# Optimization experiments

Hardware: AMD Instinct MI355X
Metric: run time of the kernel (lower is better)

Reference implementation:

```python
import jax, jax.numpy as jnp
import numpy as np

B, T, D, H = 4, 4096, 1024, 64

def setup_inputs() -> dict:
    key = jax.random.key(0)
    k1, k2, k3, k4 = jax.random.split(key, 4)
    x = jax.random.normal(k1, (B, T, D), dtype=jnp.float32)
    Wk = jax.random.normal(k2, (D, H), dtype=jnp.float32) * (D ** -0.5)
    Wq = jax.random.normal(k3, (D, H), dtype=jnp.float32) * (D ** -0.5)
    Wv = jax.random.normal(k4, (D, H), dtype=jnp.float32) * (D ** -0.5)
    return {"x": x, "Wk": Wk, "Wq": Wq, "Wv": Wv}

def reference(x, Wk, Wq, Wv):
    # single-head causal self-attention (dropout inactive: training=False)
    k = x @ Wk  # [B,T,H]
    q = x @ Wq  # [B,T,H]
    v = x @ Wv  # [B,T,H]
    scale = jnp.float32(1.0) / jnp.sqrt(jnp.float32(H))
    wei = jnp.einsum('bth,bsh->bts', q, k) * scale  # [B,T,T]
    t = x.shape[1]
    causal = jnp.tril(jnp.ones((t, t), dtype=bool))[None, :, :]
    wei = jnp.where(causal, wei, jnp.float32(-jnp.inf))
    wei = jax.nn.softmax(wei, axis=-1)
    out = jnp.einsum('bts,bsh->bth', wei, v)  # [B,T,H]
    return out
```

## Files before the change

### kernel.cpp

```cpp
#include <hip/hip_runtime.h>

typedef __bf16 bf16_t;
typedef __bf16 bf16x8 __attribute__((ext_vector_type(8)));
typedef __bf16 bf16x4 __attribute__((ext_vector_type(4)));
typedef float  f32x4  __attribute__((ext_vector_type(4)));
typedef float  f32x16 __attribute__((ext_vector_type(16)));

#define B_  4
#define T_  4096
#define H_  64
#define BT  (B_*T_)

#define QSCALE 0.1803368801111204f

#define NSLOT_PB 1088
#define NSLOT    4352

#define WS_KFR  0x0000000u
#define WS_QFR  0x0200000u
#define WS_VFR  0x0400000u
#define WS_WTF  0x0600000u
#define WS_POUT 0x0680000u
#define WS_PL   0x1780000u

#define MFMA16(a,b,c) __builtin_amdgcn_mfma_f32_16x16x32_bf16((a),(b),(c),0,0,0)
#define MFMA32(a,b,c) __builtin_amdgcn_mfma_f32_32x32x16_bf16((a),(b),(c),0,0,0)

__device__ __forceinline__ unsigned pk2(float a, float b) {
  union { __bf16 h[2]; unsigned u; } u_;
  u_.h[0] = (__bf16)a; u_.h[1] = (__bf16)b;
  return u_.u;
}

__device__ __forceinline__ f32x16 zero16() {
  f32x16 z;
#pragma unroll
  for (int i = 0; i < 16; ++i) z[i] = 0.f;
  return z;
}

__global__ __launch_bounds__(128) void wtrans_kernel(
    const float* __restrict__ Wk, const float* __restrict__ Wq,
    const float* __restrict__ Wv, bf16_t* __restrict__ WTf) {
  __shared__ float lw[64][17];
  int bid = blockIdx.x;
  int nt = bid >> 4;
  int kc = bid & 15;
  int w  = nt >> 2;
  const float* W = (w == 0) ? Wk : (w == 1) ? Wq : Wv;
  float sc = (w == 1) ? QSCALE : 1.0f;
  int nl0 = (nt & 3) * 16;

  int t = threadIdx.x;
  int rr = t >> 1;
  int c0 = (t & 1) * 8;
  const float* src = W + (size_t)(kc*64 + rr)*64 + nl0 + c0;
  float4 v0 = *reinterpret_cast<const float4*>(src);
  float4 v1 = *reinterpret_cast<const float4*>(src + 4);
  lw[rr][c0+0] = v0.x; lw[rr][c0+1] = v0.y; lw[rr][c0+2] = v0.z; lw[rr][c0+3] = v0.w;
  lw[rr][c0+4] = v1.x; lw[rr][c0+5] = v1.y; lw[rr][c0+6] = v1.z; lw[rr][c0+7] = v1.w;
  __syncthreads();

  int kk   = t >> 6;
  int lane = t & 63;
  int col  = lane & 15;
  int g    = lane >> 4;
  bf16x8 o;
#pragma unroll
  for (int e = 0; e < 8; ++e) o[e] = (bf16_t)(lw[kk*32 + g*8 + e][col] * sc);
  *reinterpret_cast<bf16x8*>(WTf + ((size_t)bid*2 + kk)*512 + lane*8) = o;
}

__global__ __launch_bounds__(256) void proj_kernel(
    const float* __restrict__ x, const bf16_t* __restrict__ WTf,
    bf16_t* __restrict__ kfr, bf16_t* __restrict__ qfr, bf16_t* __restrict__ vfr) {
  __shared__ __bf16 xs[2][16][72];
  int tid  = threadIdx.x;
  int wv   = tid >> 6;
  int lane = tid & 63;
  int col  = lane & 15;
  int g    = lane >> 4;
  int m0   = blockIdx.x * 16;

  f32x4 zero4 = {0.f, 0.f, 0.f, 0.f};
  f32x4 acc[3] = {zero4, zero4, zero4};

  int srow = tid >> 4;
  int scol = (tid & 15) * 4;
  const float* xrow = x + (size_t)(m0 + srow)*1024 + scol;

  float4 a0 = *reinterpret_cast<const float4*>(xrow);
  float4 b0 = *reinterpret_cast<const float4*>(xrow + 64);
  {
    bf16x4 pk = { (bf16_t)a0.x,(bf16_t)a0.y,(bf16_t)a0.z,(bf16_t)a0.w };
    *reinterpret_cast<bf16x4*>(&xs[0][srow][scol]) = pk;
  }

  const bf16_t* wtb = WTf + lane*8;

  for (int t = 0; t < 16; ++t) {
    __syncthreads();
    int cur = t & 1;
    if (t + 2 < 16) {
      const float* p = xrow + (t+2)*64;
      if ((t & 1) == 0) a0 = *reinterpret_cast<const float4*>(p);
      else              b0 = *reinterpret_cast<const float4*>(p);
    }
#pragma unroll
    for (int kk = 0; kk < 2; ++kk) {
      int ko = kk*32 + g*8;
      bf16x8 f0 = *(const bf16x8*)&xs[cur][col][ko];
#pragma unroll
      for (int nti = 0; nti < 3; ++nti) {
        int nt = wv*3 + nti;
        bf16x8 bfr = *(const bf16x8*)(wtb + ((size_t)(nt*16 + t)*2 + kk)*512);
        acc[nti] = MFMA16(f0, bfr, acc[nti]);
      }
    }
    if (t + 1 < 16) {
      float4 sv = ((t & 1) == 0) ? b0 : a0;
      bf16x4 pk = { (bf16_t)sv.x,(bf16_t)sv.y,(bf16_t)sv.z,(bf16_t)sv.w };
      *reinterpret_cast<bf16x4*>(&xs[cur^1][srow][scol]) = pk;
    }
  }
  int row0 = m0 + 4*g;
#pragma unroll
  for (int nti = 0; nti < 3; ++nti) {
    int n = wv*48 + nti*16 + col;
    f32x4 v = acc[nti];
    if (n < 128) {
      int h = n & 63;
      bf16_t* base = (n < 64) ? kfr : qfr;
#pragma unroll
      for (int r = 0; r < 4; ++r) {
        int t2 = row0 + r;
        size_t idx = (size_t)((t2>>6)*8 + ((t2>>5)&1)*4 + (h>>4))*512
                   + (size_t)((t2&31) + ((h>>3)&1)*32)*8 + (h&7);
        base[idx] = (bf16_t)v[r];
      }
    } else {
      int h = n - 128;
      size_t idx = (size_t)((row0>>6)*8 + ((h>>5)&1)*4 + ((row0>>4)&3))*512
                 + (size_t)((h&31) + ((row0>>3)&1)*32)*8 + (row0&7);
      bf16x4 pk = { (bf16_t)v[0], (bf16_t)v[1], (bf16_t)v[2], (bf16_t)v[3] };
      *reinterpret_cast<bf16x4*>(&vfr[idx]) = pk;
    }
  }
}

__global__ __launch_bounds__(64) void attn_kernel(
    const bf16_t* __restrict__ qfr, const bf16_t* __restrict__ kfr,
    const bf16_t* __restrict__ vfr, bf16_t* __restrict__ pout,
    float* __restrict__ pl) {
  int l  = threadIdx.x;
  int ql = l & 31;
  int hi = l >> 5;

  int bidx = blockIdx.x;
  int b = bidx / NSLOT_PB;
  int s = bidx - b * NSLOT_PB;
  s = NSLOT_PB - 1 - s;
  int a = 0;
#pragma unroll
  for (int aa = 1; aa < 16; ++aa) if (4*aa*(aa+1) <= s) a = aa;
  int r2 = s - 4*a*(a+1);
  int qd = r2 / (a+1);
  int c  = r2 - qd*(a+1);
  int jt = 8*a + qd;
  int slot = b*NSLOT_PB + s;

  int q0    = jt << 5;
  int kv_lo = c << 8;
  int kv_hi = min(kv_lo + 256, q0 + 32);
  int ntiles = (kv_hi - kv_lo + 63) >> 6;
  int qg = q0 + ql;

  const bf16_t* qb = qfr + (size_t)((b*T_ + q0) >> 6)*4096
                   + (size_t)((q0 >> 5) & 1)*2048 + l*8;
  bf16x8 qf0 = *(const bf16x8*)(qb);
  bf16x8 qf1 = *(const bf16x8*)(qb + 512);
  bf16x8 qf2 = *(const bf16x8*)(qb + 1024);
  bf16x8 qf3 = *(const bf16x8*)(qb + 1536);

  const bf16_t* kfb = kfr + (size_t)(b*T_)*64 + l*8;
  const bf16_t* vfb = vfr + (size_t)(b*T_)*64 + l*8;

  bf16x8 kA0,kA1,kA2,kA3, kB0,kB1,kB2,kB3;
#define LOADK(kvt_) do { const bf16_t* kp_ = kfb + (size_t)(kvt_)*64;          \
    kA0=*(const bf16x8*)(kp_);        kA1=*(const bf16x8*)(kp_+512);           \
    kA2=*(const bf16x8*)(kp_+1024);   kA3=*(const bf16x8*)(kp_+1536);          \
    kB0=*(const bf16x8*)(kp_+2048);   kB1=*(const bf16x8*)(kp_+2560);          \
    kB2=*(const bf16x8*)(kp_+3072);   kB3=*(const bf16x8*)(kp_+3584); } while(0)

  LOADK(kv_lo);

  f32x16 oA = zero16(), oB = zero16();
  float l_ = 0.f;

  for (int t = 0; t < ntiles; ++t) {
    int kvt = kv_lo + t*64;
    const bf16_t* vp = vfb + (size_t)kvt*64;
    bf16x8 vA0 = *(const bf16x8*)(vp);
    bf16x8 vA1 = *(const bf16x8*)(vp + 512);
    bf16x8 vA2 = *(const bf16x8*)(vp + 1024);
    bf16x8 vA3 = *(const bf16x8*)(vp + 1536);
    bf16x8 vB0 = *(const bf16x8*)(vp + 2048);
    bf16x8 vB1 = *(const bf16x8*)(vp + 2560);
    bf16x8 vB2 = *(const bf16x8*)(vp + 3072);
    bf16x8 vB3 = *(const bf16x8*)(vp + 3584);

    f32x16 sA = zero16(), sB = zero16();
    __builtin_amdgcn_s_setprio(1);
    sA = MFMA32(kA0, qf0, sA); sB = MFMA32(kB0, qf0, sB);
    sA = MFMA32(kA1, qf1, sA); sB = MFMA32(kB1, qf1, sB);
    sA = MFMA32(kA2, qf2, sA); sB = MFMA32(kB2, qf2, sB);
    sA = MFMA32(kA3, qf3, sA); sB = MFMA32(kB3, qf3, sB);
    __builtin_amdgcn_s_setprio(0);

    if (t + 1 < ntiles) LOADK(kvt + 64);

    if (kvt + 63 > q0) {
#pragma unroll
      for (int r = 0; r < 16; ++r) {
        int kvo = kvt + (r&3) + 8*(r>>2) + 4*hi;
        if (kvo > qg)      sA[r] = -1e30f;
        if (kvo + 32 > qg) sB[r] = -1e30f;
      }
    }

    float pA[16], pB[16];
    float ts = 0.f;
#pragma unroll
    for (int r = 0; r < 16; ++r) { pA[r] = exp2f(sA[r]); ts += pA[r]; }
#pragma unroll
    for (int r = 0; r < 16; ++r) { pB[r] = exp2f(sB[r]); ts += pB[r]; }
    l_ += ts + __shfl_xor(ts, 32);

    bf16x8 p0, p1, p2, p3;
#define MKSLICES(P, F0, F1) do {                                               \
    unsigned w0 = pk2(P[0],P[1]),   w1 = pk2(P[2],P[3]);                       \
    unsigned w2 = pk2(P[4],P[5]),   w3 = pk2(P[6],P[7]);                       \
    unsigned w4 = pk2(P[8],P[9]),   w5 = pk2(P[10],P[11]);                     \
    unsigned w6 = pk2(P[12],P[13]), w7 = pk2(P[14],P[15]);                     \
    unsigned x0 = (unsigned)__shfl_xor((int)w0,32);                            \
    unsigned x1 = (unsigned)__shfl_xor((int)w1,32);                            \
    unsigned x2 = (unsigned)__shfl_xor((int)w2,32);                            \
    unsigned x3 = (unsigned)__shfl_xor((int)w3,32);                            \
    unsigned x4 = (unsigned)__shfl_xor((int)w4,32);                            \
    unsigned x5 = (unsigned)__shfl_xor((int)w5,32);                            \
    unsigned x6 = (unsigned)__shfl_xor((int)w6,32);                            \
    unsigned x7 = (unsigned)__shfl_xor((int)w7,32);                            \
    union { unsigned d[4]; bf16x8 v; } u0_, u1_;                               \
    u0_.d[0] = hi ? x2 : w0;  u0_.d[1] = hi ? x3 : w1;                         \
    u0_.d[2] = hi ? w2 : x0;  u0_.d[3] = hi ? w3 : x1;                         \
    u1_.d[0] = hi ? x6 : w4;  u1_.d[1] = hi ? x7 : w5;                         \
    u1_.d[2] = hi ? w6 : x4;  u1_.d[3] = hi ? w7 : x5;                         \
    F0 = u0_.v; F1 = u1_.v; } while(0)
    MKSLICES(pA, p0, p1);
    MKSLICES(pB, p2, p3);

    __builtin_amdgcn_s_setprio(1);
    oA = MFMA32(vA0, p0, oA); oB = MFMA32(vB0, p0, oB);
    oA = MFMA32(vA1, p1, oA); oB = MFMA32(vB1, p1, oB);
    oA = MFMA32(vA2, p2, oA); oB = MFMA32(vB2, p2, oB);
    oA = MFMA32(vA3, p3, oA); oB = MFMA32(vB3, p3, oB);
    __builtin_amdgcn_s_setprio(0);
  }

  bf16_t* po = pout + (size_t)slot * 2048;
#pragma unroll
  for (int r = 0; r < 16; ++r) {
    int h = (r&3) + 8*(r>>2) + 4*hi;
    po[h*32 + ql]      = (bf16_t)oA[r];
    po[(h+32)*32 + ql] = (bf16_t)oB[r];
  }
  if (l < 32) pl[(size_t)slot*32 + l] = l_;
}

__global__ __launch_bounds__(256) void combine_kernel(
    const bf16_t* __restrict__ pout, const float* __restrict__ pl,
    float* __restrict__ out) {
  int blk = blockIdx.x;
  int b  = blk >> 7;
  int jt = blk & 127;
  int tid = threadIdx.x;
  int wv = tid >> 6;
  int l  = tid & 63;
  int a  = jt >> 3;
  int nch = a + 1;
  int slot0 = b*NSLOT_PB + 4*a*(a+1) + (jt & 7)*(a+1);

  float oacc[8], lacc[8];
#pragma unroll
  for (int q = 0; q < 8; ++q) { oacc[q] = 0.f; lacc[q] = 0.f; }
  for (int c2 = 0; c2 < nch; ++c2) {
    const bf16_t* pp = pout + (size_t)(slot0 + c2)*2048 + l*32 + wv*8;
    bf16x8 o8 = *(const bf16x8*)pp;
    const float* plc = pl + (size_t)(slot0 + c2)*32 + wv*8;
#pragma unroll
    for (int q = 0; q < 8; ++q) { oacc[q] += (float)o8[q]; lacc[q] += plc[q]; }
  }
  float* op = out + ((size_t)b*T_ + (size_t)jt*32 + wv*8)*64 + l;
#pragma unroll
  for (int q = 0; q < 8; ++q) op[(size_t)q*64] = oacc[q] / lacc[q];
}

extern "C" void kernel_launch(void* const* d_in, const int* in_sizes, int n_in,
                              void* d_out, int out_size, void* d_ws, size_t ws_size,
                              hipStream_t stream) {
  (void)in_sizes; (void)n_in; (void)out_size; (void)ws_size;
  const float* x  = (const float*)d_in[0];
  const float* Wk = (const float*)d_in[1];
  const float* Wq = (const float*)d_in[2];
  const float* Wv = (const float*)d_in[3];
  char* ws = (char*)d_ws;
  bf16_t* kfr  = (bf16_t*)(ws + WS_KFR);
  bf16_t* qfr  = (bf16_t*)(ws + WS_QFR);
  bf16_t* vfr  = (bf16_t*)(ws + WS_VFR);
  bf16_t* WTf  = (bf16_t*)(ws + WS_WTF);
  bf16_t* pout = (bf16_t*)(ws + WS_POUT);
  float*  pl   = (float*)(ws + WS_PL);
  float*  outp = (float*)d_out;

  hipLaunchKernelGGL(wtrans_kernel,  dim3(192),   dim3(128), 0, stream, Wk, Wq, Wv, WTf);
  hipLaunchKernelGGL(proj_kernel,    dim3(1024),  dim3(256), 0, stream, x, WTf, kfr, qfr, vfr);
  hipLaunchKernelGGL(attn_kernel,    dim3(NSLOT), dim3(64),  0, stream, qfr, kfr, vfr, pout, pl);
  hipLaunchKernelGGL(combine_kernel, dim3(512),   dim3(256), 0, stream, pout, pl, outp);
}
```

Baseline: 65.57 us.

## Fuse four kernels into one cooperative persistent kernel with grid syncs

Merges weight transpose, projection, attention and combine into a single cooperative kernel of 512 blocks separated by grid-wide barriers, removing three kernel launch gaps. The projection now computes 32 rows per block with prefetched weight fragments, and attention runs four waves per block looping over slots, with V loads software-pipelined one tile ahead. Risks include grid-sync cost, lower parallelism for attention (2048 waves over 4352 slots, causing tail imbalance), and register pressure from the launch bound of two blocks per CU. A fallback path launches the separate kernels if the cooperative launch fails.

```diff
diff --git a/kernel.cpp b/kernel.cpp
--- a/kernel.cpp
+++ b/kernel.cpp
@@ -1,4 +1,7 @@
 #include <hip/hip_runtime.h>
+#include <hip/hip_cooperative_groups.h>
+
+namespace cg = cooperative_groups;
 
 typedef __bf16 bf16_t;
 typedef __bf16 bf16x8 __attribute__((ext_vector_type(8)));
@@ -15,6 +18,7 @@
 
 #define NSLOT_PB 1088
 #define NSLOT    4352
+#define NWAVES   2048
 
 #define WS_KFR  0x0000000u
 #define WS_QFR  0x0200000u
@@ -26,6 +30,8 @@
 #define MFMA16(a,b,c) __builtin_amdgcn_mfma_f32_16x16x32_bf16((a),(b),(c),0,0,0)
 #define MFMA32(a,b,c) __builtin_amdgcn_mfma_f32_32x32x16_bf16((a),(b),(c),0,0,0)
 
+#define SMEM_BYTES 9216
+
 __device__ __forceinline__ unsigned pk2(float a, float b) {
   union { __bf16 h[2]; unsigned u; } u_;
   u_.h[0] = (__bf16)a; u_.h[1] = (__bf16)b;
@@ -39,11 +45,11 @@
   return z;
 }
 
-__global__ __launch_bounds__(128) void wtrans_kernel(
+__device__ void phase_wtrans(int bid, char* smem,
     const float* __restrict__ Wk, const float* __restrict__ Wq,
     const float* __restrict__ Wv, bf16_t* __restrict__ WTf) {
-  __shared__ float lw[64][17];
-  int bid = blockIdx.x;
+  if (bid >= 192) return;
+  float (*lw)[17] = (float (*)[17])smem;
   int nt = bid >> 4;
   int kc = bid & 15;
   int w  = nt >> 2;
@@ -52,191 +58,218 @@
   int nl0 = (nt & 3) * 16;
 
   int t = threadIdx.x;
-  int rr = t >> 1;
-  int c0 = (t & 1) * 8;
-  const float* src = W + (size_t)(kc*64 + rr)*64 + nl0 + c0;
-  float4 v0 = *reinterpret_cast<const float4*>(src);
-  float4 v1 = *reinterpret_cast<const float4*>(src + 4);
-  lw[rr][c0+0] = v0.x; lw[rr][c0+1] = v0.y; lw[rr][c0+2] = v0.z; lw[rr][c0+3] = v0.w;
-  lw[rr][c0+4] = v1.x; lw[rr][c0+5] = v1.y; lw[rr][c0+6] = v1.z; lw[rr][c0+7] = v1.w;
+  int rr = t >> 2, c0 = (t & 3) * 4;
+  float4 v = *reinterpret_cast<const float4*>(W + (size_t)(kc*64 + rr)*64 + nl0 + c0);
+  lw[rr][c0+0] = v.x; lw[rr][c0+1] = v.y; lw[rr][c0+2] = v.z; lw[rr][c0+3] = v.w;
   __syncthreads();
-
-  int kk   = t >> 6;
-  int lane = t & 63;
-  int col  = lane & 15;
-  int g    = lane >> 4;
-  bf16x8 o;
-#pragma unroll
-  for (int e = 0; e < 8; ++e) o[e] = (bf16_t)(lw[kk*32 + g*8 + e][col] * sc);
-  *reinterpret_cast<bf16x8*>(WTf + ((size_t)bid*2 + kk)*512 + lane*8) = o;
-}
-
-__global__ __launch_bounds__(256) void proj_kernel(
+  if (t < 128) {
+    int kk = t >> 6, lane = t & 63, col = lane & 15, g = lane >> 4;
+    bf16x8 o;
+#pragma unroll
+    for (int e = 0; e < 8; ++e) o[e] = (bf16_t)(lw[kk*32 + g*8 + e][col] * sc);
+    *reinterpret_cast<bf16x8*>(WTf + ((size_t)(nt*16 + kc)*2 + kk)*512 + lane*8) = o;
+  }
+}
+
+__device__ void phase_proj(int bid, char* smem,
     const float* __restrict__ x, const bf16_t* __restrict__ WTf,
     bf16_t* __restrict__ kfr, bf16_t* __restrict__ qfr, bf16_t* __restrict__ vfr) {
-  __shared__ __bf16 xs[2][16][72];
+  typedef __bf16 (*xs_t)[32][72];
+  xs_t xs = (xs_t)smem;
   int tid  = threadIdx.x;
   int wv   = tid >> 6;
   int lane = tid & 63;
   int col  = lane & 15;
   int g    = lane >> 4;
-  int m0   = blockIdx.x * 16;
+  int m0   = bid * 32;
 
   f32x4 zero4 = {0.f, 0.f, 0.f, 0.f};
-  f32x4 acc[3] = {zero4, zero4, zero4};
-
-  int srow = tid >> 4;
-  int scol = (tid & 15) * 4;
+  f32x4 acc[2][3];
+#pragma unroll
+  for (int i = 0; i < 2; ++i)
+#pragma unroll
+    for (int j = 0; j < 3; ++j) acc[i][j] = zero4;
+
+  int srow = tid >> 3;
+  int scol = (tid & 7) * 8;
   const float* xrow = x + (size_t)(m0 + srow)*1024 + scol;
 
   float4 a0 = *reinterpret_cast<const float4*>(xrow);
+  float4 a1 = *reinterpret_cast<const float4*>(xrow + 4);
   float4 b0 = *reinterpret_cast<const float4*>(xrow + 64);
+  float4 b1 = *reinterpret_cast<const float4*>(xrow + 68);
   {
-    bf16x4 pk = { (bf16_t)a0.x,(bf16_t)a0.y,(bf16_t)a0.z,(bf16_t)a0.w };
-    *reinterpret_cast<bf16x4*>(&xs[0][srow][scol]) = pk;
+    bf16x8 pk = { (bf16_t)a0.x,(bf16_t)a0.y,(bf16_t)a0.z,(bf16_t)a0.w,
+                  (bf16_t)a1.x,(bf16_t)a1.y,(bf16_t)a1.z,(bf16_t)a1.w };
+    *reinterpret_cast<bf16x8*>(&xs[0][srow][scol]) = pk;
   }
 
   const bf16_t* wtb = WTf + lane*8;
-
+  bf16x8 bcur[6], bnxt[6];
+#pragma unroll
+  for (int kk = 0; kk < 2; ++kk)
+#pragma unroll
+    for (int nti = 0; nti < 3; ++nti)
+      bcur[kk*3+nti] = *(const bf16x8*)(wtb + ((size_t)((wv*3+nti)*16 + 0)*2 + kk)*512);
+
+#pragma unroll
   for (int t = 0; t < 16; ++t) {
     __syncthreads();
     int cur = t & 1;
     if (t + 2 < 16) {
       const float* p = xrow + (t+2)*64;
-      if ((t & 1) == 0) a0 = *reinterpret_cast<const float4*>(p);
-      else              b0 = *reinterpret_cast<const float4*>(p);
+      if ((t & 1) == 0) { a0 = *reinterpret_cast<const float4*>(p);
+                          a1 = *reinterpret_cast<const float4*>(p + 4); }
+      else              { b0 = *reinterpret_cast<const float4*>(p);
+                          b1 = *reinterpret_cast<const float4*>(p + 4); }
+    }
+    if (t + 1 < 16) {
+#pragma unroll
+      for (int kk = 0; kk < 2; ++kk)
+#pragma unroll
+        for (int nti = 0; nti < 3; ++nti)
+          bnxt[kk*3+nti] = *(const bf16x8*)(wtb + ((size_t)((wv*3+nti)*16 + (t+1))*2 + kk)*512);
     }
 #pragma unroll
     for (int kk = 0; kk < 2; ++kk) {
       int ko = kk*32 + g*8;
-      bf16x8 f0 = *(const bf16x8*)&xs[cur][col][ko];
+      bf16x8 f0 = *(const bf16x8*)&xs[cur][ 0 + col][ko];
+      bf16x8 f1 = *(const bf16x8*)&xs[cur][16 + col][ko];
 #pragma unroll
       for (int nti = 0; nti < 3; ++nti) {
-        int nt = wv*3 + nti;
-        bf16x8 bfr = *(const bf16x8*)(wtb + ((size_t)(nt*16 + t)*2 + kk)*512);
-        acc[nti] = MFMA16(f0, bfr, acc[nti]);
+        acc[0][nti] = MFMA16(f0, bcur[kk*3+nti], acc[0][nti]);
+        acc[1][nti] = MFMA16(f1, bcur[kk*3+nti], acc[1][nti]);
       }
     }
     if (t + 1 < 16) {
-      float4 sv = ((t & 1) == 0) ? b0 : a0;
-      bf16x4 pk = { (bf16_t)sv.x,(bf16_t)sv.y,(bf16_t)sv.z,(bf16_t)sv.w };
-      *reinterpret_cast<bf16x4*>(&xs[cur^1][srow][scol]) = pk;
-    }
-  }
-  int row0 = m0 + 4*g;
-#pragma unroll
-  for (int nti = 0; nti < 3; ++nti) {
-    int n = wv*48 + nti*16 + col;
-    f32x4 v = acc[nti];
-    if (n < 128) {
-      int h = n & 63;
-      bf16_t* base = (n < 64) ? kfr : qfr;
-#pragma unroll
-      for (int r = 0; r < 4; ++r) {
-        int t2 = row0 + r;
-        size_t idx = (size_t)((t2>>6)*8 + ((t2>>5)&1)*4 + (h>>4))*512
-                   + (size_t)((t2&31) + ((h>>3)&1)*32)*8 + (h&7);
-        base[idx] = (bf16_t)v[r];
+      bf16x8 pk;
+      if ((t & 1) == 0)
+        pk = bf16x8{ (bf16_t)b0.x,(bf16_t)b0.y,(bf16_t)b0.z,(bf16_t)b0.w,
+                     (bf16_t)b1.x,(bf16_t)b1.y,(bf16_t)b1.z,(bf16_t)b1.w };
+      else
+        pk = bf16x8{ (bf16_t)a0.x,(bf16_t)a0.y,(bf16_t)a0.z,(bf16_t)a0.w,
+                     (bf16_t)a1.x,(bf16_t)a1.y,(bf16_t)a1.z,(bf16_t)a1.w };
+      *reinterpret_cast<bf16x8*>(&xs[cur^1][srow][scol]) = pk;
+    }
+#pragma unroll
+    for (int i = 0; i < 6; ++i) bcur[i] = bnxt[i];
+  }
+#pragma unroll
+  for (int mt = 0; mt < 2; ++mt) {
+    int row0 = m0 + mt*16 + 4*g;
+#pragma unroll
+    for (int nti = 0; nti < 3; ++nti) {
+      int n = wv*48 + nti*16 + col;
+      f32x4 v = acc[mt][nti];
+      if (n < 128) {
+        int h = n & 63;
+        bf16_t* base = (n < 64) ? kfr : qfr;
+#pragma unroll
+        for (int r = 0; r < 4; ++r) {
+          int t2 = row0 + r;
+          size_t idx = (size_t)((t2>>6)*8 + ((t2>>5)&1)*4 + (h>>4))*512
+                     + (size_t)((t2&31) + ((h>>3)&1)*32)*8 + (h&7);
+          base[idx] = (bf16_t)v[r];
+        }
+      } else {
+        int h = n - 128;
+        size_t idx = (size_t)((row0>>6)*8 + ((h>>5)&1)*4 + ((row0>>4)&3))*512
+                   + (size_t)((h&31) + ((row0>>3)&1)*32)*8 + (row0&7);
+        bf16x4 pk = { (bf16_t)v[0], (bf16_t)v[1], (bf16_t)v[2], (bf16_t)v[3] };
+        *reinterpret_cast<bf16x4*>(&vfr[idx]) = pk;
       }
-    } else {
-      int h = n - 128;
-      size_t idx = (size_t)((row0>>6)*8 + ((h>>5)&1)*4 + ((row0>>4)&3))*512
-                 + (size_t)((h&31) + ((row0>>3)&1)*32)*8 + (row0&7);
-      bf16x4 pk = { (bf16_t)v[0], (bf16_t)v[1], (bf16_t)v[2], (bf16_t)v[3] };
-      *reinterpret_cast<bf16x4*>(&vfr[idx]) = pk;
-    }
-  }
-}
-
-__global__ __launch_bounds__(64) void attn_kernel(
+    }
+  }
+}
+
+__device__ void phase_attn(int bid,
     const bf16_t* __restrict__ qfr, const bf16_t* __restrict__ kfr,
     const bf16_t* __restrict__ vfr, bf16_t* __restrict__ pout,
     float* __restrict__ pl) {
-  int l  = threadIdx.x;
-  int ql = l & 31;
-  int hi = l >> 5;
-
-  int bidx = blockIdx.x;
-  int b = bidx / NSLOT_PB;
-  int s = bidx - b * NSLOT_PB;
-  s = NSLOT_PB - 1 - s;
-  int a = 0;
-#pragma unroll
-  for (int aa = 1; aa < 16; ++aa) if (4*aa*(aa+1) <= s) a = aa;
-  int r2 = s - 4*a*(a+1);
-  int qd = r2 / (a+1);
-  int c  = r2 - qd*(a+1);
-  int jt = 8*a + qd;
-  int slot = b*NSLOT_PB + s;
-
-  int q0    = jt << 5;
-  int kv_lo = c << 8;
-  int kv_hi = min(kv_lo + 256, q0 + 32);
-  int ntiles = (kv_hi - kv_lo + 63) >> 6;
-  int qg = q0 + ql;
-
-  const bf16_t* qb = qfr + (size_t)((b*T_ + q0) >> 6)*4096
-                   + (size_t)((q0 >> 5) & 1)*2048 + l*8;
-  bf16x8 qf0 = *(const bf16x8*)(qb);
-  bf16x8 qf1 = *(const bf16x8*)(qb + 512);
-  bf16x8 qf2 = *(const bf16x8*)(qb + 1024);
-  bf16x8 qf3 = *(const bf16x8*)(qb + 1536);
-
-  const bf16_t* kfb = kfr + (size_t)(b*T_)*64 + l*8;
-  const bf16_t* vfb = vfr + (size_t)(b*T_)*64 + l*8;
-
-  bf16x8 kA0,kA1,kA2,kA3, kB0,kB1,kB2,kB3;
+  int tid = threadIdx.x;
+  int wv  = tid >> 6;
+  int l   = tid & 63;
+  int ql  = l & 31;
+  int hi  = l >> 5;
+
+  for (int si = bid*4 + wv; si < NSLOT; si += NWAVES) {
+    int b = si / NSLOT_PB;
+    int s = si - b * NSLOT_PB;
+    s = NSLOT_PB - 1 - s;
+    int a = 0;
+#pragma unroll
+    for (int aa = 1; aa < 16; ++aa) if (4*aa*(aa+1) <= s) a = aa;
+    int r2 = s - 4*a*(a+1);
+    int qd = r2 / (a+1);
+    int c  = r2 - qd*(a+1);
+    int jt = 8*a + qd;
+    int slot = b*NSLOT_PB + s;
+
+    int q0    = jt << 5;
+    int kv_lo = c << 8;
+    int kv_hi = min(kv_lo + 256, q0 + 32);
+    int ntiles = (kv_hi - kv_lo + 63) >> 6;
+    int qg = q0 + ql;
+
+    const bf16_t* qb = qfr + (size_t)((b*T_ + q0) >> 6)*4096
+                     + (size_t)((q0 >> 5) & 1)*2048 + l*8;
+    bf16x8 qf0 = *(const bf16x8*)(qb);
+    bf16x8 qf1 = *(const bf16x8*)(qb + 512);
+    bf16x8 qf2 = *(const bf16x8*)(qb + 1024);
+    bf16x8 qf3 = *(const bf16x8*)(qb + 1536);
+
+    const bf16_t* kfb = kfr + (size_t)(b*T_)*64 + l*8;
+    const bf16_t* vfb = vfr + (size_t)(b*T_)*64 + l*8;
+
+    bf16x8 kA0,kA1,kA2,kA3, kB0,kB1,kB2,kB3;
+    bf16x8 vA0,vA1,vA2,vA3, vB0,vB1,vB2,vB3;
 #define LOADK(kvt_) do { const bf16_t* kp_ = kfb + (size_t)(kvt_)*64;          \
     kA0=*(const bf16x8*)(kp_);        kA1=*(const bf16x8*)(kp_+512);           \
     kA2=*(const bf16x8*)(kp_+1024);   kA3=*(const bf16x8*)(kp_+1536);          \
     kB0=*(const bf16x8*)(kp_+2048);   kB1=*(const bf16x8*)(kp_+2560);          \
     kB2=*(const bf16x8*)(kp_+3072);   kB3=*(const bf16x8*)(kp_+3584); } while(0)
-
-  LOADK(kv_lo);
-
-  f32x16 oA = zero16(), oB = zero16();
-  float l_ = 0.f;
-
-  for (int t = 0; t < ntiles; ++t) {
-    int kvt = kv_lo + t*64;
-    const bf16_t* vp = vfb + (size_t)kvt*64;
-    bf16x8 vA0 = *(const bf16x8*)(vp);
-    bf16x8 vA1 = *(const bf16x8*)(vp + 512);
-    bf16x8 vA2 = *(const bf16x8*)(vp + 1024);
-    bf16x8 vA3 = *(const bf16x8*)(vp + 1536);
-    bf16x8 vB0 = *(const bf16x8*)(vp + 2048);
-    bf16x8 vB1 = *(const bf16x8*)(vp + 2560);
-    bf16x8 vB2 = *(const bf16x8*)(vp + 3072);
-    bf16x8 vB3 = *(const bf16x8*)(vp + 3584);
-
-    f32x16 sA = zero16(), sB = zero16();
-    __builtin_amdgcn_s_setprio(1);
-    sA = MFMA32(kA0, qf0, sA); sB = MFMA32(kB0, qf0, sB);
-    sA = MFMA32(kA1, qf1, sA); sB = MFMA32(kB1, qf1, sB);
-    sA = MFMA32(kA2, qf2, sA); sB = MFMA32(kB2, qf2, sB);
-    sA = MFMA32(kA3, qf3, sA); sB = MFMA32(kB3, qf3, sB);
-    __builtin_amdgcn_s_setprio(0);
-
-    if (t + 1 < ntiles) LOADK(kvt + 64);
-
-    if (kvt + 63 > q0) {
-#pragma unroll
-      for (int r = 0; r < 16; ++r) {
-        int kvo = kvt + (r&3) + 8*(r>>2) + 4*hi;
-        if (kvo > qg)      sA[r] = -1e30f;
-        if (kvo + 32 > qg) sB[r] = -1e30f;
+#define LOADV(kvt_) do { const bf16_t* vp_ = vfb + (size_t)(kvt_)*64;          \
+    vA0=*(const bf16x8*)(vp_);        vA1=*(const bf16x8*)(vp_+512);           \
+    vA2=*(const bf16x8*)(vp_+1024);   vA3=*(const bf16x8*)(vp_+1536);          \
+    vB0=*(const bf16x8*)(vp_+2048);   vB1=*(const bf16x8*)(vp_+2560);          \
+    vB2=*(const bf16x8*)(vp_+3072);   vB3=*(const bf16x8*)(vp_+3584); } while(0)
+
+    LOADK(kv_lo);
+    LOADV(kv_lo);
+
+    f32x16 oA = zero16(), oB = zero16();
+    float l_ = 0.f;
+
+    for (int t = 0; t < ntiles; ++t) {
+      int kvt = kv_lo + t*64;
+      f32x16 sA = zero16(), sB = zero16();
+      __builtin_amdgcn_s_setprio(1);
+      sA = MFMA32(kA0, qf0, sA); sB = MFMA32(kB0, qf0, sB);
+      sA = MFMA32(kA1, qf1, sA); sB = MFMA32(kB1, qf1, sB);
+      sA = MFMA32(kA2, qf2, sA); sB = MFMA32(kB2, qf2, sB);
+      sA = MFMA32(kA3, qf3, sA); sB = MFMA32(kB3, qf3, sB);
+      __builtin_amdgcn_s_setprio(0);
+
+      if (t + 1 < ntiles) LOADK(kvt + 64);
+
+      if (kvt + 63 > q0) {
+#pragma unroll
+        for (int r = 0; r < 16; ++r) {
+          int kvo = kvt + (r&3) + 8*(r>>2) + 4*hi;
+          if (kvo > qg)      sA[r] = -1e30f;
+          if (kvo + 32 > qg) sB[r] = -1e30f;
+        }
       }
-    }
-
-    float pA[16], pB[16];
-    float ts = 0.f;
-#pragma unroll
-    for (int r = 0; r < 16; ++r) { pA[r] = exp2f(sA[r]); ts += pA[r]; }
-#pragma unroll
-    for (int r = 0; r < 16; ++r) { pB[r] = exp2f(sB[r]); ts += pB[r]; }
-    l_ += ts + __shfl_xor(ts, 32);
-
-    bf16x8 p0, p1, p2, p3;
+
+      float pA[16], pB[16];
+      float ts = 0.f;
+#pragma unroll
+      for (int r = 0; r < 16; ++r) { pA[r] = exp2f(sA[r]); ts += pA[r]; }
+#pragma unroll
+      for (int r = 0; r < 16; ++r) { pB[r] = exp2f(sB[r]); ts += pB[r]; }
+      l_ += ts + __shfl_xor(ts, 32);
+
+      bf16x8 p0, p1, p2, p3;
 #define MKSLICES(P, F0, F1) do {                                               \
     unsigned w0 = pk2(P[0],P[1]),   w1 = pk2(P[2],P[3]);                       \
     unsigned w2 = pk2(P[4],P[5]),   w3 = pk2(P[6],P[7]);                       \
@@ -256,33 +289,37 @@
     u1_.d[0] = hi ? x6 : w4;  u1_.d[1] = hi ? x7 : w5;                         \
     u1_.d[2] = hi ? w6 : x4;  u1_.d[3] = hi ? w7 : x5;                         \
     F0 = u0_.v; F1 = u1_.v; } while(0)
-    MKSLICES(pA, p0, p1);
-    MKSLICES(pB, p2, p3);
-
-    __builtin_amdgcn_s_setprio(1);
-    oA = MFMA32(vA0, p0, oA); oB = MFMA32(vB0, p0, oB);
-    oA = MFMA32(vA1, p1, oA); oB = MFMA32(vB1, p1, oB);
-    oA = MFMA32(vA2, p2, oA); oB = MFMA32(vB2, p2, oB);
-    oA = MFMA32(vA3, p3, oA); oB = MFMA32(vB3, p3, oB);
-    __builtin_amdgcn_s_setprio(0);
-  }
-
-  bf16_t* po = pout + (size_t)slot * 2048;
-#pragma unroll
-  for (int r = 0; r < 16; ++r) {
-    int h = (r&3) + 8*(r>>2) + 4*hi;
-    po[h*32 + ql]      = (bf16_t)oA[r];
-    po[(h+32)*32 + ql] = (bf16_t)oB[r];
-  }
-  if (l < 32) pl[(size_t)slot*32 + l] = l_;
-}
-
-__global__ __launch_bounds__(256) void combine_kernel(
+      MKSLICES(pA, p0, p1);
+      MKSLICES(pB, p2, p3);
+
+      __builtin_amdgcn_s_setprio(1);
+      oA = MFMA32(vA0, p0, oA); oB = MFMA32(vB0, p0, oB);
+      oA = MFMA32(vA1, p1, oA); oB = MFMA32(vB1, p1, oB);
+      oA = MFMA32(vA2, p2, oA); oB = MFMA32(vB2, p2, oB);
+      oA = MFMA32(vA3, p3, oA); oB = MFMA32(vB3, p3, oB);
+      __builtin_amdgcn_s_setprio(0);
+
+      if (t + 1 < ntiles) LOADV(kvt + 64);
+    }
+
+    bf16_t* po = pout + (size_t)slot * 2048;
+#pragma unroll
+    for (int r = 0; r < 16; ++r) {
+      int h = (r&3) + 8*(r>>2) + 4*hi;
+      po[h*32 + ql]      = (bf16_t)oA[r];
+      po[(h+32)*32 + ql] = (bf16_t)oB[r];
+    }
+    if (l < 32) pl[(size_t)slot*32 + l] = l_;
+  }
+#undef LOADK
+#undef LOADV
+}
+
+__device__ void phase_combine(int bid,
     const bf16_t* __restrict__ pout, const float* __restrict__ pl,
     float* __restrict__ out) {
-  int blk = blockIdx.x;
-  int b  = blk >> 7;
-  int jt = blk & 127;
+  int b  = bid >> 7;
+  int jt = bid & 127;
   int tid = threadIdx.x;
   int wv = tid >> 6;
   int l  = tid & 63;
@@ -303,6 +340,52 @@
   float* op = out + ((size_t)b*T_ + (size_t)jt*32 + wv*8)*64 + l;
 #pragma unroll
   for (int q = 0; q < 8; ++q) op[(size_t)q*64] = oacc[q] / lacc[q];
+}
+
+__global__ __launch_bounds__(256, 2) void fused_kernel(
+    const float* __restrict__ x, const float* __restrict__ Wk,
+    const float* __restrict__ Wq, const float* __restrict__ Wv,
+    char* __restrict__ ws, float* __restrict__ out) {
+  __shared__ __align__(16) char smem[SMEM_BYTES];
+  bf16_t* kfr  = (bf16_t*)(ws + WS_KFR);
+  bf16_t* qfr  = (bf16_t*)(ws + WS_QFR);
+  bf16_t* vfr  = (bf16_t*)(ws + WS_VFR);
+  bf16_t* WTf  = (bf16_t*)(ws + WS_WTF);
+  bf16_t* pout = (bf16_t*)(ws + WS_POUT);
+  float*  pl   = (float*)(ws + WS_PL);
+  int bid = blockIdx.x;
+
+  phase_wtrans(bid, smem, Wk, Wq, Wv, WTf);
+  cg::this_grid().sync();
+  phase_proj(bid, smem, x, WTf, kfr, qfr, vfr);
+  cg::this_grid().sync();
+  phase_attn(bid, qfr, kfr, vfr, pout, pl);
+  cg::this_grid().sync();
+  phase_combine(bid, pout, pl, out);
+}
+
+__global__ __launch_bounds__(256) void wtrans_kernel(
+    const float* __restrict__ Wk, const float* __restrict__ Wq,
+    const float* __restrict__ Wv, bf16_t* __restrict__ WTf) {
+  __shared__ __align__(16) char smem[SMEM_BYTES];
+  phase_wtrans(blockIdx.x, smem, Wk, Wq, Wv, WTf);
+}
+__global__ __launch_bounds__(256) void proj_kernel(
+    const float* __restrict__ x, const bf16_t* __restrict__ WTf,
+    bf16_t* __restrict__ kfr, bf16_t* __restrict__ qfr, bf16_t* __restrict__ vfr) {
+  __shared__ __align__(16) char smem[SMEM_BYTES];
+  phase_proj(blockIdx.x, smem, x, WTf, kfr, qfr, vfr);
+}
+__global__ __launch_bounds__(256) void attn_kernel(
+    const bf16_t* __restrict__ qfr, const bf16_t* __restrict__ kfr,
+    const bf16_t* __restrict__ vfr, bf16_t* __restrict__ pout,
+    float* __restrict__ pl) {
+  phase_attn(blockIdx.x, qfr, kfr, vfr, pout, pl);
+}
+__global__ __launch_bounds__(256) void combine_kernel(
+    const bf16_t* __restrict__ pout, const float* __restrict__ pl,
+    float* __restrict__ out) {
+  phase_combine(blockIdx.x, pout, pl, out);
 }
 
 extern "C" void kernel_launch(void* const* d_in, const int* in_sizes, int n_in,
@@ -313,17 +396,23 @@
   const float* Wk = (const float*)d_in[1];
   const float* Wq = (const float*)d_in[2];
   const float* Wv = (const float*)d_in[3];
-  char* ws = (char*)d_ws;
-  bf16_t* kfr  = (bf16_t*)(ws + WS_KFR);
-  bf16_t* qfr  = (bf16_t*)(ws + WS_QFR);
-  bf16_t* vfr  = (bf16_t*)(ws + WS_VFR);
-  bf16_t* WTf  = (bf16_t*)(ws + WS_WTF);
-  bf16_t* pout = (bf16_t*)(ws + WS_POUT);
-  float*  pl   = (float*)(ws + WS_PL);
-  float*  outp = (float*)d_out;
-
-  hipLaunchKernelGGL(wtrans_kernel,  dim3(192),   dim3(128), 0, stream, Wk, Wq, Wv, WTf);
-  hipLaunchKernelGGL(proj_kernel,    dim3(1024),  dim3(256), 0, stream, x, WTf, kfr, qfr, vfr);
-  hipLaunchKernelGGL(attn_kernel,    dim3(NSLOT), dim3(64),  0, stream, qfr, kfr, vfr, pout, pl);
-  hipLaunchKernelGGL(combine_kernel, dim3(512),   dim3(256), 0, stream, pout, pl, outp);
-}
+  char*  ws   = (char*)d_ws;
+  float* outp = (float*)d_out;
+
+  void* args[6] = { (void*)&x, (void*)&Wk, (void*)&Wq, (void*)&Wv,
+                    (void*)&ws, (void*)&outp };
+  hipError_t e = hipLaunchCooperativeKernel((const void*)fused_kernel,
+                                            dim3(512), dim3(256), args, 0, stream);
+  if (e != hipSuccess) {
+    bf16_t* kfr  = (bf16_t*)(ws + WS_KFR);
+    bf16_t* qfr  = (bf16_t*)(ws + WS_QFR);
+    bf16_t* vfr  = (bf16_t*)(ws + WS_VFR);
+    bf16_t* WTf  = (bf16_t*)(ws + WS_WTF);
+    bf16_t* pout = (bf16_t*)(ws + WS_POUT);
+    float*  pl   = (float*)(ws + WS_PL);
+    hipLaunchKernelGGL(wtrans_kernel,  dim3(192), dim3(256), 0, stream, Wk, Wq, Wv, WTf);
+    hipLaunchKernelGGL(proj_kernel,    dim3(512), dim3(256), 0, stream, x, WTf, kfr, qfr, vfr);
+    hipLaunchKernelGGL(attn_kernel,    dim3(512), dim3(256), 0, stream, qfr, kfr, vfr, pout, pl);
+    hipLaunchKernelGGL(combine_kernel, dim3(512), dim3(256), 0, stream, pout, pl, outp);
+  }
+}
```

After: 257.6 us. 293% more time.

## Double projection row tile to 32 and prefetch weight fragments into registers

Applied to the files above, without the earlier changes.

The projection kernel now handles 32 rows per block instead of 16, so each weight fragment loaded from global memory feeds two MFMAs and weight traffic is halved. Weight fragments for the next K step are prefetched into registers while the current step computes, and the loop is fully unrolled. The grid shrinks from 1024 to 512 blocks. This raises register use and lowers the number of blocks available to fill the GPU.

```diff
diff --git a/kernel.cpp b/kernel.cpp
--- a/kernel.cpp
+++ b/kernel.cpp
@@ -74,76 +74,109 @@
 __global__ __launch_bounds__(256) void proj_kernel(
     const float* __restrict__ x, const bf16_t* __restrict__ WTf,
     bf16_t* __restrict__ kfr, bf16_t* __restrict__ qfr, bf16_t* __restrict__ vfr) {
-  __shared__ __bf16 xs[2][16][72];
+  __shared__ __bf16 xs[2][32][72];
   int tid  = threadIdx.x;
   int wv   = tid >> 6;
   int lane = tid & 63;
   int col  = lane & 15;
   int g    = lane >> 4;
-  int m0   = blockIdx.x * 16;
+  int m0   = blockIdx.x * 32;
 
   f32x4 zero4 = {0.f, 0.f, 0.f, 0.f};
-  f32x4 acc[3] = {zero4, zero4, zero4};
-
-  int srow = tid >> 4;
-  int scol = (tid & 15) * 4;
+  f32x4 acc[2][3];
+#pragma unroll
+  for (int i = 0; i < 2; ++i)
+#pragma unroll
+    for (int j = 0; j < 3; ++j) acc[i][j] = zero4;
+
+  int srow = tid >> 3;
+  int scol = (tid & 7) * 8;
   const float* xrow = x + (size_t)(m0 + srow)*1024 + scol;
 
   float4 a0 = *reinterpret_cast<const float4*>(xrow);
+  float4 a1 = *reinterpret_cast<const float4*>(xrow + 4);
   float4 b0 = *reinterpret_cast<const float4*>(xrow + 64);
+  float4 b1 = *reinterpret_cast<const float4*>(xrow + 68);
   {
-    bf16x4 pk = { (bf16_t)a0.x,(bf16_t)a0.y,(bf16_t)a0.z,(bf16_t)a0.w };
-    *reinterpret_cast<bf16x4*>(&xs[0][srow][scol]) = pk;
+    bf16x8 pk = { (bf16_t)a0.x,(bf16_t)a0.y,(bf16_t)a0.z,(bf16_t)a0.w,
+                  (bf16_t)a1.x,(bf16_t)a1.y,(bf16_t)a1.z,(bf16_t)a1.w };
+    *reinterpret_cast<bf16x8*>(&xs[0][srow][scol]) = pk;
   }
 
   const bf16_t* wtb = WTf + lane*8;
-
+  bf16x8 bcur[6], bnxt[6];
+#pragma unroll
+  for (int kk = 0; kk < 2; ++kk)
+#pragma unroll
+    for (int nti = 0; nti < 3; ++nti)
+      bcur[kk*3+nti] = *(const bf16x8*)(wtb + ((size_t)((wv*3+nti)*16 + 0)*2 + kk)*512);
+
+#pragma unroll
   for (int t = 0; t < 16; ++t) {
     __syncthreads();
     int cur = t & 1;
     if (t + 2 < 16) {
       const float* p = xrow + (t+2)*64;
-      if ((t & 1) == 0) a0 = *reinterpret_cast<const float4*>(p);
-      else              b0 = *reinterpret_cast<const float4*>(p);
+      if ((t & 1) == 0) { a0 = *reinterpret_cast<const float4*>(p);
+                          a1 = *reinterpret_cast<const float4*>(p + 4); }
+      else              { b0 = *reinterpret_cast<const float4*>(p);
+                          b1 = *reinterpret_cast<const float4*>(p + 4); }
+    }
+    if (t + 1 < 16) {
+#pragma unroll
+      for (int kk = 0; kk < 2; ++kk)
+#pragma unroll
+        for (int nti = 0; nti < 3; ++nti)
+          bnxt[kk*3+nti] = *(const bf16x8*)(wtb + ((size_t)((wv*3+nti)*16 + (t+1))*2 + kk)*512);
     }
 #pragma unroll
     for (int kk = 0; kk < 2; ++kk) {
       int ko = kk*32 + g*8;
-      bf16x8 f0 = *(const bf16x8*)&xs[cur][col][ko];
+      bf16x8 f0 = *(const bf16x8*)&xs[cur][ 0 + col][ko];
+      bf16x8 f1 = *(const bf16x8*)&xs[cur][16 + col][ko];
 #pragma unroll
       for (int nti = 0; nti < 3; ++nti) {
-        int nt = wv*3 + nti;
-        bf16x8 bfr = *(const bf16x8*)(wtb + ((size_t)(nt*16 + t)*2 + kk)*512);
-        acc[nti] = MFMA16(f0, bfr, acc[nti]);
+        acc[0][nti] = MFMA16(f0, bcur[kk*3+nti], acc[0][nti]);
+        acc[1][nti] = MFMA16(f1, bcur[kk*3+nti], acc[1][nti]);
       }
     }
     if (t + 1 < 16) {
-      float4 sv = ((t & 1) == 0) ? b0 : a0;
-      bf16x4 pk = { (bf16_t)sv.x,(bf16_t)sv.y,(bf16_t)sv.z,(bf16_t)sv.w };
-      *reinterpret_cast<bf16x4*>(&xs[cur^1][srow][scol]) = pk;
-    }
-  }
-  int row0 = m0 + 4*g;
-#pragma unroll
-  for (int nti = 0; nti < 3; ++nti) {
-    int n = wv*48 + nti*16 + col;
-    f32x4 v = acc[nti];
-    if (n < 128) {
-      int h = n & 63;
-      bf16_t* base = (n < 64) ? kfr : qfr;
-#pragma unroll
-      for (int r = 0; r < 4; ++r) {
-        int t2 = row0 + r;
-        size_t idx = (size_t)((t2>>6)*8 + ((t2>>5)&1)*4 + (h>>4))*512
-                   + (size_t)((t2&31) + ((h>>3)&1)*32)*8 + (h&7);
-        base[idx] = (bf16_t)v[r];
+      bf16x8 pk;
+      if ((t & 1) == 0)
+        pk = bf16x8{ (bf16_t)b0.x,(bf16_t)b0.y,(bf16_t)b0.z,(bf16_t)b0.w,
+                     (bf16_t)b1.x,(bf16_t)b1.y,(bf16_t)b1.z,(bf16_t)b1.w };
+      else
+        pk = bf16x8{ (bf16_t)a0.x,(bf16_t)a0.y,(bf16_t)a0.z,(bf16_t)a0.w,
+                     (bf16_t)a1.x,(bf16_t)a1.y,(bf16_t)a1.z,(bf16_t)a1.w };
+      *reinterpret_cast<bf16x8*>(&xs[cur^1][srow][scol]) = pk;
+    }
+#pragma unroll
+    for (int i = 0; i < 6; ++i) bcur[i] = bnxt[i];
+  }
+#pragma unroll
+  for (int mt = 0; mt < 2; ++mt) {
+    int row0 = m0 + mt*16 + 4*g;
+#pragma unroll
+    for (int nti = 0; nti < 3; ++nti) {
+      int n = wv*48 + nti*16 + col;
+      f32x4 v = acc[mt][nti];
+      if (n < 128) {
+        int h = n & 63;
+        bf16_t* base = (n < 64) ? kfr : qfr;
+#pragma unroll
+        for (int r = 0; r < 4; ++r) {
+          int t2 = row0 + r;
+          size_t idx = (size_t)((t2>>6)*8 + ((t2>>5)&1)*4 + (h>>4))*512
+                     + (size_t)((t2&31) + ((h>>3)&1)*32)*8 + (h&7);
+          base[idx] = (bf16_t)v[r];
+        }
+      } else {
+        int h = n - 128;
+        size_t idx = (size_t)((row0>>6)*8 + ((h>>5)&1)*4 + ((row0>>4)&3))*512
+                   + (size_t)((h&31) + ((row0>>3)&1)*32)*8 + (row0&7);
+        bf16x4 pk = { (bf16_t)v[0], (bf16_t)v[1], (bf16_t)v[2], (bf16_t)v[3] };
+        *reinterpret_cast<bf16x4*>(&vfr[idx]) = pk;
       }
-    } else {
-      int h = n - 128;
-      size_t idx = (size_t)((row0>>6)*8 + ((h>>5)&1)*4 + ((row0>>4)&3))*512
-                 + (size_t)((h&31) + ((row0>>3)&1)*32)*8 + (row0&7);
-      bf16x4 pk = { (bf16_t)v[0], (bf16_t)v[1], (bf16_t)v[2], (bf16_t)v[3] };
-      *reinterpret_cast<bf16x4*>(&vfr[idx]) = pk;
     }
   }
 }
@@ -323,7 +356,7 @@
   float*  outp = (float*)d_out;
 
   hipLaunchKernelGGL(wtrans_kernel,  dim3(192),   dim3(128), 0, stream, Wk, Wq, Wv, WTf);
-  hipLaunchKernelGGL(proj_kernel,    dim3(1024),  dim3(256), 0, stream, x, WTf, kfr, qfr, vfr);
+  hipLaunchKernelGGL(proj_kernel,    dim3(512),   dim3(256), 0, stream, x, WTf, kfr, qfr, vfr);
   hipLaunchKernelGGL(attn_kernel,    dim3(NSLOT), dim3(64),  0, stream, qfr, kfr, vfr, pout, pl);
   hipLaunchKernelGGL(combine_kernel, dim3(512),   dim3(256), 0, stream, pout, pl, outp);
 }
```

Result: faster. 57.88 us (median of 2 runs) (-11.7%).

## Load projection inputs straight into MFMA fragments, dropping LDS staging

Applied to the files above, without the earlier changes.

The projection kernel no longer stages x through shared memory with per-step barriers. Each wave now reads its fp32 x rows directly in MFMA A-fragment layout, converts them to bf16 in registers, and keeps a two-deep register prefetch of both x and weight fragments. Each block now covers 32 rows with 6 output tiles per wave, and the grid is halved, with a launch-bounds occupancy hint added. This removes LDS traffic and synchronisation from a bandwidth-bound pass, at the cost of higher register pressure and less coalesced global x reads.

```diff
diff --git a/kernel.cpp b/kernel.cpp
--- a/kernel.cpp
+++ b/kernel.cpp
@@ -71,62 +71,61 @@
   *reinterpret_cast<bf16x8*>(WTf + ((size_t)bid*2 + kk)*512 + lane*8) = o;
 }
 
-__global__ __launch_bounds__(256) void proj_kernel(
+__global__ __launch_bounds__(256, 3) void proj_kernel(
     const float* __restrict__ x, const bf16_t* __restrict__ WTf,
     bf16_t* __restrict__ kfr, bf16_t* __restrict__ qfr, bf16_t* __restrict__ vfr) {
-  __shared__ __bf16 xs[2][16][72];
   int tid  = threadIdx.x;
   int wv   = tid >> 6;
   int lane = tid & 63;
   int col  = lane & 15;
   int g    = lane >> 4;
-  int m0   = blockIdx.x * 16;
+  int m0   = blockIdx.x * 32 + (wv >> 1) * 16;
+  int ch   = wv & 1;
 
   f32x4 zero4 = {0.f, 0.f, 0.f, 0.f};
-  f32x4 acc[3] = {zero4, zero4, zero4};
-
-  int srow = tid >> 4;
-  int scol = (tid & 15) * 4;
-  const float* xrow = x + (size_t)(m0 + srow)*1024 + scol;
-
-  float4 a0 = *reinterpret_cast<const float4*>(xrow);
-  float4 b0 = *reinterpret_cast<const float4*>(xrow + 64);
-  {
-    bf16x4 pk = { (bf16_t)a0.x,(bf16_t)a0.y,(bf16_t)a0.z,(bf16_t)a0.w };
-    *reinterpret_cast<bf16x4*>(&xs[0][srow][scol]) = pk;
-  }
-
-  const bf16_t* wtb = WTf + lane*8;
-
-  for (int t = 0; t < 16; ++t) {
-    __syncthreads();
-    int cur = t & 1;
-    if (t + 2 < 16) {
-      const float* p = xrow + (t+2)*64;
-      if ((t & 1) == 0) a0 = *reinterpret_cast<const float4*>(p);
-      else              b0 = *reinterpret_cast<const float4*>(p);
+  f32x4 acc[6] = {zero4, zero4, zero4, zero4, zero4, zero4};
+
+  const float*  xp  = x + (size_t)(m0 + col)*1024 + g*8;
+  const bf16_t* wtb = WTf + (size_t)(ch*6)*32*512 + lane*8;
+
+  float4 xa[2][2];
+  bf16x8 bfr[2][6];
+#pragma unroll
+  for (int s = 0; s < 2; ++s) {
+    xa[s][0] = *reinterpret_cast<const float4*>(xp + s*32);
+    xa[s][1] = *reinterpret_cast<const float4*>(xp + s*32 + 4);
+#pragma unroll
+    for (int n = 0; n < 6; ++n)
+      bfr[s][n] = *(const bf16x8*)(wtb + ((size_t)n*32 + s)*512);
+  }
+
+#pragma unroll
+  for (int j = 0; j < 32; ++j) {
+    const int s = j & 1;
+    float4 u0 = xa[s][0], u1 = xa[s][1];
+    bf16x8 b0 = bfr[s][0], b1 = bfr[s][1], b2 = bfr[s][2],
+           b3 = bfr[s][3], b4 = bfr[s][4], b5 = bfr[s][5];
+    if (j + 2 < 32) {
+      xa[s][0] = *reinterpret_cast<const float4*>(xp + (j+2)*32);
+      xa[s][1] = *reinterpret_cast<const float4*>(xp + (j+2)*32 + 4);
+#pragma unroll
+      for (int n = 0; n < 6; ++n)
+        bfr[s][n] = *(const bf16x8*)(wtb + ((size_t)n*32 + j + 2)*512);
     }
-#pragma unroll
-    for (int kk = 0; kk < 2; ++kk) {
-      int ko = kk*32 + g*8;
-      bf16x8 f0 = *(const bf16x8*)&xs[cur][col][ko];
-#pragma unroll
-      for (int nti = 0; nti < 3; ++nti) {
-        int nt = wv*3 + nti;
-        bf16x8 bfr = *(const bf16x8*)(wtb + ((size_t)(nt*16 + t)*2 + kk)*512);
-        acc[nti] = MFMA16(f0, bfr, acc[nti]);
-      }
-    }
-    if (t + 1 < 16) {
-      float4 sv = ((t & 1) == 0) ? b0 : a0;
-      bf16x4 pk = { (bf16_t)sv.x,(bf16_t)sv.y,(bf16_t)sv.z,(bf16_t)sv.w };
-      *reinterpret_cast<bf16x4*>(&xs[cur^1][srow][scol]) = pk;
-    }
-  }
+    bf16x8 af = { (bf16_t)u0.x,(bf16_t)u0.y,(bf16_t)u0.z,(bf16_t)u0.w,
+                  (bf16_t)u1.x,(bf16_t)u1.y,(bf16_t)u1.z,(bf16_t)u1.w };
+    acc[0] = MFMA16(af, b0, acc[0]);
+    acc[1] = MFMA16(af, b1, acc[1]);
+    acc[2] = MFMA16(af, b2, acc[2]);
+    acc[3] = MFMA16(af, b3, acc[3]);
+    acc[4] = MFMA16(af, b4, acc[4]);
+    acc[5] = MFMA16(af, b5, acc[5]);
+  }
+
   int row0 = m0 + 4*g;
 #pragma unroll
-  for (int nti = 0; nti < 3; ++nti) {
-    int n = wv*48 + nti*16 + col;
+  for (int nti = 0; nti < 6; ++nti) {
+    int n = ch*96 + nti*16 + col;
     f32x4 v = acc[nti];
     if (n < 128) {
       int h = n & 63;
@@ -323,7 +322,7 @@
   float*  outp = (float*)d_out;
 
   hipLaunchKernelGGL(wtrans_kernel,  dim3(192),   dim3(128), 0, stream, Wk, Wq, Wv, WTf);
-  hipLaunchKernelGGL(proj_kernel,    dim3(1024),  dim3(256), 0, stream, x, WTf, kfr, qfr, vfr);
+  hipLaunchKernelGGL(proj_kernel,    dim3(512),   dim3(256), 0, stream, x, WTf, kfr, qfr, vfr);
   hipLaunchKernelGGL(attn_kernel,    dim3(NSLOT), dim3(64),  0, stream, qfr, kfr, vfr, pout, pl);
   hipLaunchKernelGGL(combine_kernel, dim3(512),   dim3(256), 0, stream, pout, pl, outp);
 }
```

After: 78.29 us. +19.4%, slower.
